# Kernel optimization log

Measured on AMD Instinct MI355X. Metric: run time of the kernel, lower is better.

The kernel has to match this reference:

```python
import jax, jax.numpy as jnp
import numpy as np

T = 8
TAU = 2.0       # spikingjelly LIFNode default tau
VTH = 1.0       # default v_threshold
ALPHA = 2.0     # surrogate.ATan alpha
EPS = 1e-5      # BatchNorm eps


@jax.custom_vjp
def spike_fn(x):
    # Heaviside with ATan surrogate gradient
    return (x >= 0.0).astype(x.dtype)

def _spike_fwd(x):
    return (x >= 0.0).astype(x.dtype), x

def _spike_bwd(x, g):
    sg = (ALPHA / 2.0) / (1.0 + (jnp.pi / 2.0 * ALPHA * x) ** 2)
    return (g * sg,)

spike_fn.defvjp(_spike_fwd, _spike_bwd)


def lif(x_seq):
    """Multi-step LIF over leading time axis. decay_input=True, hard reset to 0, detach_reset."""
    def step(v, x):
        v = v + (x - v) / TAU            # charge
        s = spike_fn(v - VTH)            # fire (surrogate grad)
        v = v * (1.0 - jax.lax.stop_gradient(s))  # detached hard reset to v_reset=0
        return v, s
    _, s_seq = jax.lax.scan(step, jnp.zeros_like(x_seq[0]), x_seq)
    return s_seq


def conv2d(x, w, b, stride):
    y = jax.lax.conv_general_dilated(x, w, (stride, stride), 'VALID',
                                     dimension_numbers=('NCHW', 'OIHW', 'NCHW'))
    return y + b[None, :, None, None]


def batchnorm(x, g, b):
    # training-mode BN over merged (T*B, H, W) axes, matching step_mode='m' BatchNorm2d
    m = x.mean((0, 2, 3), keepdims=True)
    v = x.var((0, 2, 3), keepdims=True)
    return g[None, :, None, None] * (x - m) * jax.lax.rsqrt(v + EPS) + b[None, :, None, None]


def setup_inputs() -> dict:
    key = jax.random.key(0)
    ks = jax.random.split(key, 12)
    def w_init(k, shape):
        fan_in = int(np.prod(shape[1:]))
        return jax.random.normal(k, shape, dtype=jnp.float32) / np.sqrt(fan_in)
    x = jax.random.normal(ks[0], (128, 4, 84, 84), dtype=jnp.float32)
    return {
        'x': x,
        'conv1_w': w_init(ks[1], (32, 4, 8, 8)),  'conv1_b': jnp.zeros((32,), jnp.float32),
        'bn1_g': jnp.ones((32,), jnp.float32),    'bn1_b': jnp.zeros((32,), jnp.float32),
        'conv2_w': w_init(ks[2], (64, 32, 4, 4)), 'conv2_b': jnp.zeros((64,), jnp.float32),
        'bn2_g': jnp.ones((64,), jnp.float32),    'bn2_b': jnp.zeros((64,), jnp.float32),
        'conv3_w': w_init(ks[3], (64, 64, 3, 3)), 'conv3_b': jnp.zeros((64,), jnp.float32),
        'bn3_g': jnp.ones((64,), jnp.float32),    'bn3_b': jnp.zeros((64,), jnp.float32),
        'fc1_w': w_init(ks[4], (512, 3136)),      'fc1_b': jnp.zeros((512,), jnp.float32),
        'fco_w': w_init(ks[5], (2, 512)),         'fco_b': jnp.zeros((2,), jnp.float32),
    }


def reference(x, conv1_w, conv1_b, bn1_g, bn1_b, conv2_w, conv2_b, bn2_g, bn2_b,
              conv3_w, conv3_b, bn3_g, bn3_b, fc1_w, fc1_b, fco_w, fco_b):
    B = x.shape[0]
    # replicate input over T timesteps; fold T into batch for conv/BN (step_mode='m')
    xs = jnp.broadcast_to(x, (T,) + x.shape).reshape((T * B,) + x.shape[1:])

    h = batchnorm(conv2d(xs, conv1_w, conv1_b, 4), bn1_g, bn1_b)   # [TB,32,20,20]
    s = lif(h.reshape((T, B) + h.shape[1:]))
    h = s.reshape((T * B,) + s.shape[2:])

    h = batchnorm(conv2d(h, conv2_w, conv2_b, 2), bn2_g, bn2_b)    # [TB,64,9,9]
    s = lif(h.reshape((T, B) + h.shape[1:]))
    h = s.reshape((T * B,) + s.shape[2:])

    h = batchnorm(conv2d(h, conv3_w, conv3_b, 1), bn3_g, bn3_b)    # [TB,64,7,7]
    s = lif(h.reshape((T, B) + h.shape[1:]))                        # [T,B,64,7,7]

    feat = s.reshape(T, B, -1)                                      # [T,B,3136]
    hid = lif(jnp.einsum('tbi,oi->tbo', feat, fc1_w) + fc1_b)       # [T,B,512]
    out_seq = jnp.einsum('tbo,ko->tbk', hid, fco_w) + fco_b         # [T,B,2]
    return out_seq.mean(0)                                          # [B,2]
```

## Files before the change

### kernel.cpp

```cpp
#include <hip/hip_runtime.h>
#include <cstdint>
#include <cstddef>

#define TT 8

#define E2_ELEMS (128*64*81)
#define E3_ELEMS (128*64*49)

typedef __attribute__((ext_vector_type(8))) short short8;
typedef __attribute__((ext_vector_type(4))) float f32x4;

__global__ void prep_all(const float* __restrict__ w1, const float* __restrict__ w2,
                         const float* __restrict__ w3, float* __restrict__ wT1,
                         __bf16* __restrict__ w2f, __bf16* __restrict__ w3f) {
  int i = blockIdx.x * 256 + threadIdx.x;
  if (i < 8192) {
    int oc = i >> 8, pos = i & 255;
    wT1[(oc >> 4) * 4096 + pos * 16 + (oc & 15)] = w1[oc * 256 + pos];
  } else if (i < 106496) {
    int v = i - 8192;
    int j    = v & 7;
    int oc   = (v >> 3) & 63;
    int quad = (v >> 9) & 3;
    int ksg  = (v >> 11) & 15;
    int term = v >> 15;
    int k = ksg * 32 + quad * 8 + j;
    int ci = k >> 4, kpos = k & 15;
    float w = w2[oc * 512 + ci * 16 + kpos];
    float hf = (float)(__bf16)w;
    float r1 = w - hf;
    float mf = (float)(__bf16)r1;
    float r2 = r1 - mf;
    w2f[v] = (term == 0) ? (__bf16)w : (term == 1) ? (__bf16)r1 : (__bf16)r2;
  } else if (i < 217088) {
    int v = i - 106496;
    int j    = v & 7;
    int oc   = (v >> 3) & 63;
    int quad = (v >> 9) & 3;
    int tk   = v >> 11;
    int term = tk / 18, kstep = tk % 18;
    int k = kstep * 32 + quad * 8 + j;
    int pos = k >> 6, ci = k & 63;
    float w = w3[oc * 576 + ci * 9 + pos];
    float hf = (float)(__bf16)w;
    float r1 = w - hf;
    float mf = (float)(__bf16)r1;
    float r2 = r1 - mf;
    w3f[v] = (term == 0) ? (__bf16)w : (term == 1) ? (__bf16)r1 : (__bf16)r2;
  }
}

__global__ __launch_bounds__(256) void prep_wff(const float* __restrict__ w,
                                                __bf16* __restrict__ wf) {
  __shared__ float tile[12544];
  int oc0 = blockIdx.x * 32;
  int ci0 = blockIdx.y * 8;
  int tid = threadIdx.x;
  for (int f = tid; f < 12544; f += 256) {
    int oc_l = f / 392, r = f - oc_l * 392;
    tile[f] = w[(size_t)(oc0 + oc_l) * 3136 + ci0 * 49 + r];
  }
  __syncthreads();
  int squad = (ci0 & 31) >> 3;
  int sadd  = ci0 >> 5;
  for (int g = tid; g < 1568; g += 256) {
    int pos = g >> 5, oc_l = g & 31;
    union { __bf16 h[8]; uint4 u; } T0, T1, T2;
    #pragma unroll
    for (int j = 0; j < 8; j++) {
      float wv = tile[oc_l * 392 + j * 49 + pos];
      float hf = (float)(__bf16)wv;
      float r1 = wv - hf;
      float mf = (float)(__bf16)r1;
      float r2 = r1 - mf;
      T0.h[j] = (__bf16)wv; T1.h[j] = (__bf16)r1; T2.h[j] = (__bf16)r2;
    }
    int s = pos * 2 + sadd;
    size_t b0 = (((size_t)s * 4 + squad) * 512 + oc0 + oc_l) * 8;
    *(uint4*)(wf + b0)           = T0.u;
    *(uint4*)(wf + b0 + 1605632) = T1.u;
    *(uint4*)(wf + b0 + 3211264) = T2.u;
  }
}

__global__ __launch_bounds__(128) void k_conv1(const float* __restrict__ x,
                                               const float* __restrict__ wT,
                                               const float* __restrict__ bias,
                                               float* __restrict__ out,
                                               float* __restrict__ pout) {
  __shared__ float xt[8064];
  int tid = threadIdx.x;
  int img = blockIdx.x >> 2;
  int q   = blockIdx.x & 3;
  int och = blockIdx.y;
  float4* dst = (float4*)xt;
  #pragma unroll
  for (int ci = 0; ci < 4; ci++) {
    const float4* s4 = (const float4*)(x + (size_t)img * 28224 + ci * 7056 + q * 1680);
    for (int i = tid; i < 504; i += 128) dst[ci * 504 + i] = s4[i];
  }
  __syncthreads();
  bool active = tid < 100;
  int oyl = tid / 20, ox = tid % 20;
  float acc[16];
  #pragma unroll
  for (int j = 0; j < 16; j++) acc[j] = 0.f;
  if (active) {
    int xb0 = oyl * 336 + ox * 4;
    const float* wh = wT + och * 4096;
    #pragma unroll 1
    for (int ci = 0; ci < 4; ci++) {
      #pragma unroll 1
      for (int ky = 0; ky < 8; ky++) {
        const float* xr = xt + ci * 2016 + xb0 + ky * 84;
        float4 xa  = *(const float4*)xr;
        float4 xbv = *(const float4*)(xr + 4);
        const float* wr = wh + (ci * 8 + ky) * 128;
        float xs[8] = {xa.x, xa.y, xa.z, xa.w, xbv.x, xbv.y, xbv.z, xbv.w};
        #pragma unroll
        for (int kx = 0; kx < 8; kx++) {
          #pragma unroll
          for (int j = 0; j < 16; j++)
            acc[j] = fmaf(xs[kx], wr[kx * 16 + j], acc[j]);
        }
      }
    }
  }
  __syncthreads();
  size_t obase = (size_t)img * 12800 + och * 6400 + (q * 5 + oyl) * 20 + ox;
  #pragma unroll
  for (int j = 0; j < 16; j++) {
    float v = 0.f;
    if (active) {
      v = acc[j] + bias[och * 16 + j];
      out[obase + j * 400] = v;
    }
    xt[j * 128 + tid] = v;
    xt[2048 + j * 128 + tid] = v * v;
  }
  __syncthreads();
  for (int off = 64; off > 0; off >>= 1) {
    if (tid < off) {
      #pragma unroll
      for (int j = 0; j < 16; j++) {
        xt[j * 128 + tid] += xt[j * 128 + tid + off];
        xt[2048 + j * 128 + tid] += xt[2048 + j * 128 + tid + off];
      }
    }
    __syncthreads();
  }
  if (tid < 16) {
    pout[(och * 16 + tid) * 512 + blockIdx.x] = xt[tid * 128];
    pout[16384 + (och * 16 + tid) * 512 + blockIdx.x] = xt[2048 + tid * 128];
  }
}

__global__ void k_bnfinal2(const float* __restrict__ pin, int sqoff, float n,
                           float* __restrict__ meanArr, float* __restrict__ rstdArr) {
  __shared__ float l0[256], l1[256];
  int c = blockIdx.x, tid = threadIdx.x;
  l0[tid] = pin[c * 512 + tid] + pin[c * 512 + tid + 256];
  l1[tid] = pin[sqoff + c * 512 + tid] + pin[sqoff + c * 512 + tid + 256];
  __syncthreads();
  for (int k = 128; k > 0; k >>= 1) {
    if (tid < k) { l0[tid] += l0[tid + k]; l1[tid] += l1[tid + k]; }
    __syncthreads();
  }
  if (tid == 0) {
    float m = l0[0] / n;
    float var = l1[0] / n - m * m;
    meanArr[c] = m;
    rstdArr[c] = rsqrtf(var + 1e-5f);
  }
}

__global__ void k_lif1b(const float* __restrict__ h, const float* __restrict__ mean,
                        const float* __restrict__ rstd, const float* __restrict__ g,
                        const float* __restrict__ bb, uint32_t* __restrict__ sout) {
  int idx = blockIdx.x * 256 + threadIdx.x;
  int ic = idx / 20;
  int ci = ic & 31;
  const float* hp = h + (size_t)idx * 20;
  float gm = g[ci], mm = mean[ci], rs = rstd[ci], bc = bb[ci];
  float xv[20];
  #pragma unroll
  for (int j4 = 0; j4 < 5; j4++) {
    float4 hv = ((const float4*)hp)[j4];
    xv[j4 * 4 + 0] = gm * (hv.x - mm) * rs + bc;
    xv[j4 * 4 + 1] = gm * (hv.y - mm) * rs + bc;
    xv[j4 * 4 + 2] = gm * (hv.z - mm) * rs + bc;
    xv[j4 * 4 + 3] = gm * (hv.w - mm) * rs + bc;
  }
  float v[20];
  #pragma unroll
  for (int j = 0; j < 20; j++) v[j] = 0.f;
  #pragma unroll
  for (int t = 0; t < TT; t++) {
    uint32_t w = 0;
    #pragma unroll
    for (int j = 0; j < 20; j++) {
      v[j] = v[j] + (xv[j] - v[j]) * 0.5f;
      uint32_t s = (v[j] >= 1.0f);
      w |= s << j;
      if (s) v[j] = 0.f;
    }
    sout[t * 81920 + idx] = w;
  }
}

__global__ __launch_bounds__(256) void k_conv2m(const uint32_t* __restrict__ s1b,
                                                const __bf16* __restrict__ wf,
                                                const float* __restrict__ bias,
                                                float* __restrict__ out,
                                                float* __restrict__ pout) {
  __shared__ uint32_t sp[1280];
  __shared__ uint4 wl4[3072];
  __bf16* wl = (__bf16*)wl4;
  int tid = threadIdx.x;
  int img0 = blockIdx.x * 2;
  {
    const uint32_t* src = s1b + (size_t)img0 * 640;
    for (int i = tid; i < 1280; i += 256) sp[i] = src[i];
  }
  int wave = tid >> 6, lane = tid & 63;
  int img_local = wave >> 1;
  int nh = wave & 1;
  int l15 = lane & 15, quad = lane >> 4;
  int ci_off = quad >> 1;
  int kyp = (quad & 1) * 2;
  int spb[6], sh[6];
  #pragma unroll
  for (int mt = 0; mt < 6; mt++) {
    int px = mt * 16 + l15;
    if (px > 80) px = 80;
    int oy = px / 9, ox = px - oy * 9;
    sh[mt]  = ox * 2;
    spb[mt] = img_local * 640 + ci_off * 20 + oy * 2 + kyp;
  }
  f32x4 acc[6][2];
  #pragma unroll
  for (int mt = 0; mt < 6; mt++)
    #pragma unroll
    for (int nt = 0; nt < 2; nt++) acc[mt][nt] = (f32x4){0.f, 0.f, 0.f, 0.f};

  for (int kc = 0; kc < 4; kc++) {
    __syncthreads();
    for (int o = tid * 8; o < 24576; o += 2048) {
      int tk = o >> 11;
      int term = tk >> 2, ksl = tk & 3;
      const __bf16* src = wf + (((term * 16 + kc * 4 + ksl)) << 11) + (o & 2047);
      *(uint4*)(wl + o) = *(const uint4*)src;
    }
    __syncthreads();
    #pragma unroll
    for (int ks = 0; ks < 4; ks++) {
      int ksg = kc * 4 + ks;
      short8 a[6];
      #pragma unroll
      for (int mt = 0; mt < 6; mt++) {
        uint32_t w0 = sp[spb[mt] + ksg * 40];
        uint32_t w1 = sp[spb[mt] + ksg * 40 + 1];
        uint32_t n0 = (w0 >> sh[mt]) & 15u;
        uint32_t n1 = (w1 >> sh[mt]) & 15u;
        union { uint32_t u[4]; short8 v; } A;
        A.u[0] = ((n0 & 1u) ? 0x3F80u : 0u) | ((n0 & 2u) ? 0x3F800000u : 0u);
        A.u[1] = ((n0 & 4u) ? 0x3F80u : 0u) | ((n0 & 8u) ? 0x3F800000u : 0u);
        A.u[2] = ((n1 & 1u) ? 0x3F80u : 0u) | ((n1 & 2u) ? 0x3F800000u : 0u);
        A.u[3] = ((n1 & 4u) ? 0x3F80u : 0u) | ((n1 & 8u) ? 0x3F800000u : 0u);
        a[mt] = A.v;
      }
      #pragma unroll
      for (int term = 0; term < 3; term++) {
        int fb = ((term * 4 + ks) << 11) + (quad << 9);
        #pragma unroll
        for (int nt = 0; nt < 2; nt++) {
          short8 b = *(const short8*)(wl + fb + ((((nh << 1) | nt) << 4) + l15) * 8);
          #pragma unroll
          for (int mt = 0; mt < 6; mt++)
            acc[mt][nt] = __builtin_amdgcn_mfma_f32_16x16x32_bf16(a[mt], b, acc[mt][nt], 0, 0, 0);
        }
      }
    }
  }
  float sl[2], sl2[2];
  #pragma unroll
  for (int nt = 0; nt < 2; nt++) {
    sl[nt] = 0.f; sl2[nt] = 0.f;
    int oc = nh * 32 + nt * 16 + l15;
    float bv = bias[oc];
    float* op = out + ((size_t)(img0 + img_local) * 64 + oc) * 81;
    #pragma unroll
    for (int mt = 0; mt < 6; mt++) {
      int pxr = mt * 16 + quad * 4;
      #pragma unroll
      for (int r = 0; r < 4; r++) {
        int px = pxr + r;
        if (px < 81) {
          float v = acc[mt][nt][r] + bv;
          op[px] = v;
          sl[nt] += v; sl2[nt] += v * v;
        }
      }
    }
  }
  __syncthreads();
  float* sred = (float*)wl4;
  #pragma unroll
  for (int nt = 0; nt < 2; nt++) {
    int oc = nh * 32 + nt * 16 + l15;
    int idx = oc * 8 + img_local * 4 + quad;
    sred[idx] = sl[nt];
    sred[512 + idx] = sl2[nt];
  }
  __syncthreads();
  if (tid < 64) {
    float s = 0.f, s2 = 0.f;
    #pragma unroll
    for (int k = 0; k < 8; k++) { s += sred[tid * 8 + k]; s2 += sred[512 + tid * 8 + k]; }
    pout[tid * 512 + blockIdx.x] = s;
    pout[32768 + tid * 512 + blockIdx.x] = s2;
  }
}

__global__ __launch_bounds__(256) void k_lifb2T(const float* __restrict__ h,
                                                const float* __restrict__ mean,
                                                const float* __restrict__ rstd,
                                                const float* __restrict__ g,
                                                const float* __restrict__ bb,
                                                uint32_t* __restrict__ s2T) {
  __shared__ uint32_t sb[288];
  int b = blockIdx.x, half = blockIdx.y;
  int tid = threadIdx.x;
  int c1 = half * 32 + tid / 9, py1 = tid % 9;
  bool has2 = tid < 32;
  int r2 = tid + 256;
  int c2i = half * 32 + r2 / 9, py2 = r2 % 9;
  float gm1 = g[c1], mm1 = mean[c1], rs1 = rstd[c1], bc1 = bb[c1];
  float gm2 = 0.f, mm2 = 0.f, rs2 = 0.f, bc2 = 0.f;
  if (has2) { gm2 = g[c2i]; mm2 = mean[c2i]; rs2 = rstd[c2i]; bc2 = bb[c2i]; }
  float v1[9], v2[9];
  #pragma unroll
  for (int j = 0; j < 9; j++) { v1[j] = 0.f; v2[j] = 0.f; }
  size_t base1 = ((size_t)b * 64 + c1) * 81 + py1 * 9;
  size_t base2 = has2 ? ((size_t)b * 64 + c2i) * 81 + py2 * 9 : base1;
  #pragma unroll 1
  for (int t = 0; t < TT; t++) {
    const float* hp = h + (size_t)t * E2_ELEMS;
    uint32_t w = 0;
    #pragma unroll
    for (int j = 0; j < 9; j++) {
      float xv = gm1 * (hp[base1 + j] - mm1) * rs1 + bc1;
      v1[j] = v1[j] + (xv - v1[j]) * 0.5f;
      uint32_t s = (v1[j] >= 1.0f);
      w |= s << j;
      if (s) v1[j] = 0.f;
    }
    sb[tid] = w;
    if (has2) {
      uint32_t w2 = 0;
      #pragma unroll
      for (int j = 0; j < 9; j++) {
        float xv = gm2 * (hp[base2 + j] - mm2) * rs2 + bc2;
        v2[j] = v2[j] + (xv - v2[j]) * 0.5f;
        uint32_t s = (v2[j] >= 1.0f);
        w2 |= s << j;
        if (s) v2[j] = 0.f;
      }
      sb[r2] = w2;
    }
    __syncthreads();
    if (tid < 81) {
      int r = tid / 9, cpix = tid - r * 9;
      uint32_t wo = 0;
      #pragma unroll
      for (int ci = 0; ci < 32; ci++)
        wo |= ((sb[ci * 9 + r] >> cpix) & 1u) << ci;
      s2T[(size_t)(t * 128 + b) * 162 + tid * 2 + half] = wo;
    }
    __syncthreads();
  }
}

__global__ __launch_bounds__(256) void k_conv3m(const uint32_t* __restrict__ s2T,
                                                const __bf16* __restrict__ wf,
                                                const float* __restrict__ bias,
                                                float* __restrict__ out,
                                                float* __restrict__ pout) {
  __shared__ uint32_t sp[324];
  __shared__ uint4 wl4[4608];
  __bf16* wl = (__bf16*)wl4;
  int tid = threadIdx.x;
  int img0 = blockIdx.x * 2;
  {
    const uint32_t* src = s2T + (size_t)img0 * 162;
    for (int i = tid; i < 324; i += 256) sp[i] = src[i];
  }
  int wave = tid >> 6, lane = tid & 63;
  int img_local = wave >> 1, nh = wave & 1;
  int l15 = lane & 15, quad = lane >> 4;
  int qsh = quad * 8;
  int base[4];
  #pragma unroll
  for (int mt = 0; mt < 4; mt++) {
    int px = mt * 16 + l15;
    if (px > 48) px = 48;
    int oy = px / 7, ox = px - oy * 7;
    base[mt] = img_local * 162 + (oy * 9 + ox) * 2;
  }
  f32x4 acc[4][2];
  #pragma unroll
  for (int mt = 0; mt < 4; mt++)
    #pragma unroll
    for (int nt = 0; nt < 2; nt++) acc[mt][nt] = (f32x4){0.f, 0.f, 0.f, 0.f};

  #pragma unroll
  for (int kc = 0; kc < 3; kc++) {
    __syncthreads();
    #pragma unroll
    for (int it = 0; it < 18; it++) {
      const __bf16* s = wf + (((it / 6) * 18 + kc * 6 + (it % 6)) << 11) + tid * 8;
      *(uint4*)(wl + (it << 11) + tid * 8) = *(const uint4*)s;
    }
    __syncthreads();
    #pragma unroll
    for (int ksl = 0; ksl < 6; ksl++) {
      int kstep = kc * 6 + ksl;
      int pos = kstep >> 1, cihalf = kstep & 1;
      int ky = pos / 3, kx = pos % 3;
      short8 a[4];
      #pragma unroll
      for (int mt = 0; mt < 4; mt++) {
        uint32_t word = sp[base[mt] + (ky * 9 + kx) * 2 + cihalf];
        uint32_t byt = (word >> qsh) & 255u;
        union { uint32_t u[4]; short8 v; } A;
        A.u[0] = ((byt & 1u)  ? 0x3F80u : 0u) | ((byt & 2u)   ? 0x3F800000u : 0u);
        A.u[1] = ((byt & 4u)  ? 0x3F80u : 0u) | ((byt & 8u)   ? 0x3F800000u : 0u);
        A.u[2] = ((byt & 16u) ? 0x3F80u : 0u) | ((byt & 32u)  ? 0x3F800000u : 0u);
        A.u[3] = ((byt & 64u) ? 0x3F80u : 0u) | ((byt & 128u) ? 0x3F800000u : 0u);
        a[mt] = A.v;
      }
      #pragma unroll
      for (int term = 0; term < 3; term++) {
        int fb = ((term * 6 + ksl) << 11) + (quad << 9);
        #pragma unroll
        for (int nt = 0; nt < 2; nt++) {
          short8 b = *(const short8*)(wl + fb + ((((nh << 1) | nt) << 4) + l15) * 8);
          #pragma unroll
          for (int mt = 0; mt < 4; mt++)
            acc[mt][nt] = __builtin_amdgcn_mfma_f32_16x16x32_bf16(a[mt], b, acc[mt][nt], 0, 0, 0);
        }
      }
    }
  }
  float sl[2], sl2[2];
  #pragma unroll
  for (int nt = 0; nt < 2; nt++) {
    sl[nt] = 0.f; sl2[nt] = 0.f;
    int oc = nh * 32 + nt * 16 + l15;
    float bv = bias[oc];
    float* op = out + ((size_t)(img0 + img_local) * 64 + oc) * 49;
    #pragma unroll
    for (int mt = 0; mt < 4; mt++) {
      int pxr = mt * 16 + quad * 4;
      #pragma unroll
      for (int r = 0; r < 4; r++) {
        int px = pxr + r;
        if (px < 49) {
          float v = acc[mt][nt][r] + bv;
          op[px] = v;
          sl[nt] += v; sl2[nt] += v * v;
        }
      }
    }
  }
  __syncthreads();
  float* sred = (float*)wl4;
  #pragma unroll
  for (int nt = 0; nt < 2; nt++) {
    int oc = nh * 32 + nt * 16 + l15;
    int idx = oc * 8 + img_local * 4 + quad;
    sred[idx] = sl[nt];
    sred[512 + idx] = sl2[nt];
  }
  __syncthreads();
  if (tid < 64) {
    float s = 0.f, s2 = 0.f;
    #pragma unroll
    for (int k = 0; k < 8; k++) { s += sred[tid * 8 + k]; s2 += sred[512 + tid * 8 + k]; }
    pout[tid * 512 + blockIdx.x] = s;
    pout[32768 + tid * 512 + blockIdx.x] = s2;
  }
}

__global__ __launch_bounds__(256) void k_lifb3T(const float* __restrict__ h,
                                                const float* __restrict__ mean,
                                                const float* __restrict__ rstd,
                                                const float* __restrict__ g,
                                                const float* __restrict__ bb,
                                                uint32_t* __restrict__ s3T) {
  __shared__ uint32_t sb[224];
  int b = blockIdx.x, half = blockIdx.y;
  int tid = threadIdx.x;
  bool active = tid < 224;
  int row = active ? tid : 0;
  int c = half * 32 + row / 7, py = row % 7;
  float gm = g[c], mm = mean[c], rs = rstd[c], bc = bb[c];
  float v[7];
  #pragma unroll
  for (int j = 0; j < 7; j++) v[j] = 0.f;
  size_t base = ((size_t)b * 64 + c) * 49 + py * 7;
  #pragma unroll 1
  for (int t = 0; t < TT; t++) {
    const float* hp = h + (size_t)t * E3_ELEMS;
    if (active) {
      uint32_t w = 0;
      #pragma unroll
      for (int j = 0; j < 7; j++) {
        float xv = gm * (hp[base + j] - mm) * rs + bc;
        v[j] = v[j] + (xv - v[j]) * 0.5f;
        uint32_t s = (v[j] >= 1.0f);
        w |= s << j;
        if (s) v[j] = 0.f;
      }
      sb[tid] = w;
    }
    __syncthreads();
    if (tid < 49) {
      int py2 = tid / 7, px = tid - py2 * 7;
      uint32_t wo = 0;
      #pragma unroll
      for (int ci = 0; ci < 32; ci++)
        wo |= ((sb[ci * 7 + py2] >> px) & 1u) << ci;
      s3T[(size_t)(t * 128 + b) * 98 + tid * 2 + half] = wo;
    }
    __syncthreads();
  }
}

__global__ __launch_bounds__(256) void k_fc1m(const uint32_t* __restrict__ s3T,
                                              const __bf16* __restrict__ wf,
                                              float* __restrict__ part) {
  __shared__ uint32_t aS[6272];
  int tid = threadIdx.x;
  int row0 = blockIdx.x * 64;
  int oc0  = blockIdx.y * 32;
  {
    const uint32_t* src = s3T + (size_t)row0 * 98;
    for (int i = tid; i < 6272; i += 256) aS[i] = src[i];
  }
  __syncthreads();
  int wave = tid >> 6, lane = tid & 63;
  int l15 = lane & 15, quad = lane >> 4;
  int qsh = quad * 8;
  f32x4 acc[4][2];
  #pragma unroll
  for (int mt = 0; mt < 4; mt++)
    #pragma unroll
    for (int nt = 0; nt < 2; nt++) acc[mt][nt] = (f32x4){0.f, 0.f, 0.f, 0.f};
  int nIter = (wave < 2) ? 25 : 24;
  #pragma unroll 1
  for (int i = 0; i < nIter; i++) {
    int ks = i * 4 + wave;
    short8 a[4];
    #pragma unroll
    for (int mt = 0; mt < 4; mt++) {
      uint32_t word = aS[(mt * 16 + l15) * 98 + ks];
      uint32_t byt = (word >> qsh) & 255u;
      union { uint32_t u[4]; short8 v; } A;
      A.u[0] = ((byt & 1u)  ? 0x3F80u : 0u) | ((byt & 2u)   ? 0x3F800000u : 0u);
      A.u[1] = ((byt & 4u)  ? 0x3F80u : 0u) | ((byt & 8u)   ? 0x3F800000u : 0u);
      A.u[2] = ((byt & 16u) ? 0x3F80u : 0u) | ((byt & 32u)  ? 0x3F800000u : 0u);
      A.u[3] = ((byt & 64u) ? 0x3F80u : 0u) | ((byt & 128u) ? 0x3F800000u : 0u);
      a[mt] = A.v;
    }
    #pragma unroll
    for (int term = 0; term < 3; term++) {
      size_t fb = ((size_t)((term * 98 + ks) * 4 + quad) * 512 + oc0 + l15) * 8;
      #pragma unroll
      for (int nt = 0; nt < 2; nt++) {
        short8 b = *(const short8*)(wf + fb + nt * 128);
        #pragma unroll
        for (int mt = 0; mt < 4; mt++)
          acc[mt][nt] = __builtin_amdgcn_mfma_f32_16x16x32_bf16(a[mt], b, acc[mt][nt], 0, 0, 0);
      }
    }
  }
  #pragma unroll
  for (int mt = 0; mt < 4; mt++) {
    #pragma unroll
    for (int nt = 0; nt < 2; nt++) {
      int oc = oc0 + nt * 16 + l15;
      #pragma unroll
      for (int r = 0; r < 4; r++) {
        int row = row0 + mt * 16 + quad * 4 + r;
        part[(size_t)wave * 524288 + (size_t)row * 512 + oc] = acc[mt][nt][r];
      }
    }
  }
}

__global__ __launch_bounds__(256) void k_fc1fco(const float* __restrict__ part,
                                                const float* __restrict__ bias,
                                                const float* __restrict__ w,
                                                const float* __restrict__ fcob,
                                                float* __restrict__ out) {
  int b = blockIdx.x, tid = threadIdx.x;
  int o0 = tid, o1 = tid + 256;
  float bv0 = bias[o0], bv1 = bias[o1];
  float v0 = 0.f, v1 = 0.f;
  float a0 = 0.f, a1 = 0.f;
  #pragma unroll
  for (int t = 0; t < TT; t++) {
    int idx0 = t * 65536 + b * 512 + o0;
    float s0 = part[idx0];
    #pragma unroll
    for (int j = 1; j < 4; j++) s0 += part[(size_t)j * 524288 + idx0];
    s0 += bv0;
    v0 = v0 + (s0 - v0) * 0.5f;
    bool sp0 = (v0 >= 1.0f);
    if (sp0) v0 = 0.f;
    int idx1 = idx0 + 256;
    float s1 = part[idx1];
    #pragma unroll
    for (int j = 1; j < 4; j++) s1 += part[(size_t)j * 524288 + idx1];
    s1 += bv1;
    v1 = v1 + (s1 - v1) * 0.5f;
    bool sp1 = (v1 >= 1.0f);
    if (sp1) v1 = 0.f;
    if (sp0) { a0 += w[o0]; a1 += w[512 + o0]; }
    if (sp1) { a0 += w[o1]; a1 += w[512 + o1]; }
  }
  __shared__ float l0[256], l1[256];
  l0[tid] = a0; l1[tid] = a1; __syncthreads();
  for (int k = 128; k > 0; k >>= 1) {
    if (tid < k) { l0[tid] += l0[tid + k]; l1[tid] += l1[tid + k]; }
    __syncthreads();
  }
  if (tid == 0) {
    out[b * 2 + 0] = l0[0] * 0.125f + fcob[0];
    out[b * 2 + 1] = l1[0] * 0.125f + fcob[1];
  }
}

extern "C" void kernel_launch(void* const* d_in, const int* in_sizes, int n_in,
                              void* d_out, int out_size, void* d_ws, size_t ws_size,
                              hipStream_t stream) {
  const float* x    = (const float*)d_in[0];
  const float* c1w  = (const float*)d_in[1];
  const float* c1b  = (const float*)d_in[2];
  const float* bn1g = (const float*)d_in[3];
  const float* bn1b = (const float*)d_in[4];
  const float* c2w  = (const float*)d_in[5];
  const float* c2b  = (const float*)d_in[6];
  const float* bn2g = (const float*)d_in[7];
  const float* bn2b = (const float*)d_in[8];
  const float* c3w  = (const float*)d_in[9];
  const float* c3b  = (const float*)d_in[10];
  const float* bn3g = (const float*)d_in[11];
  const float* bn3b = (const float*)d_in[12];
  const float* fc1w = (const float*)d_in[13];
  const float* fc1b = (const float*)d_in[14];
  const float* fcow = (const float*)d_in[15];
  const float* fcob = (const float*)d_in[16];
  float* out = (float*)d_out;

  char* ws = (char*)d_ws;
  float*    h1     = (float*)(ws + 0);
  uint32_t* s1bits = (uint32_t*)(ws + 6553600);
  float*    h2     = (float*)(ws + 19660800);
  float*    h3     = (float*)(ws + 46202880);
  __bf16*   w2f    = (__bf16*)(ws + 60882944);
  __bf16*   w3f    = (__bf16*)(ws + 61079552);
  uint32_t* s2T    = (uint32_t*)(ws + 61300736);
  float*    wT1    = (float*)(ws + 62390272);
  float*    st     = (float*)(ws + 64880640);
  __bf16*   wff    = (__bf16*)(ws + 67108864);
  float*    f1part = (float*)(ws + 76742656);
  uint32_t* s3T    = (uint32_t*)(ws + 85131264);
  float*    bnpart = (float*)(ws + 85532672);

  prep_all   <<<848, 256, 0, stream>>>(c1w, c2w, c3w, wT1, w2f, w3f);
  prep_wff   <<<dim3(16, 8), 256, 0, stream>>>(fc1w, wff);
  k_conv1    <<<dim3(512, 2), 128, 0, stream>>>(x, wT1, c1b, h1, bnpart);
  k_bnfinal2 <<<32, 256, 0, stream>>>(bnpart, 16384, 51200.f, st, st + 32);
  k_lif1b    <<<320, 256, 0, stream>>>(h1, st, st + 32, bn1g, bn1b, s1bits);

  k_conv2m   <<<512, 256, 0, stream>>>(s1bits, w2f, c2b, h2, bnpart);
  k_bnfinal2 <<<64, 256, 0, stream>>>(bnpart, 32768, 82944.f, st + 64, st + 128);
  k_lifb2T   <<<dim3(128, 2), 256, 0, stream>>>(h2, st + 64, st + 128, bn2g, bn2b, s2T);

  k_conv3m   <<<512, 256, 0, stream>>>(s2T, w3f, c3b, h3, bnpart);
  k_bnfinal2 <<<64, 256, 0, stream>>>(bnpart, 32768, 50176.f, st + 192, st + 256);
  k_lifb3T   <<<dim3(128, 2), 256, 0, stream>>>(h3, st + 192, st + 256, bn3g, bn3b, s3T);

  k_fc1m     <<<dim3(16, 16), 256, 0, stream>>>(s3T, wff, f1part);
  k_fc1fco   <<<128, 256, 0, stream>>>(f1part, fc1b, fcow, fcob, out);
}
```

Before: 251.1 us.

## Use direct global-to-LDS loads, prefetch LIF inputs, reduce fc1 partials in-block

The conv2 and conv3 weight staging now uses global_load_lds, so data goes straight into LDS without passing through registers. The LIF kernels for layers 2 and 3 prefetch the next timestep's activations into registers and use a lighter barrier macro. fc1 now splits output channels into 16-wide tiles across twice as many blocks and sums the four waves' partial results in shared memory. It writes one summed tensor instead of four partial buffers, so the final kernel reads less and uses weights held in registers. These changes add register pressure and more fc1 blocks that re-read the A tile.

```diff
diff --git a/kernel.cpp b/kernel.cpp
--- a/kernel.cpp
+++ b/kernel.cpp
@@ -9,6 +9,14 @@
 
 typedef __attribute__((ext_vector_type(8))) short short8;
 typedef __attribute__((ext_vector_type(4))) float f32x4;
+
+#define BAR_LDS() do { asm volatile("s_waitcnt lgkmcnt(0)" ::: "memory"); \
+                       __builtin_amdgcn_s_barrier(); } while (0)
+
+__device__ __forceinline__ void gld_lds16(const void* g, void* l) {
+  __builtin_amdgcn_global_load_lds((const __attribute__((address_space(1))) void*)g,
+                                   (__attribute__((address_space(3))) void*)l, 16, 0, 0);
+}
 
 __global__ void prep_all(const float* __restrict__ w1, const float* __restrict__ w2,
                          const float* __restrict__ w3, float* __restrict__ wT1,
@@ -249,7 +257,7 @@
       int tk = o >> 11;
       int term = tk >> 2, ksl = tk & 3;
       const __bf16* src = wf + (((term * 16 + kc * 4 + ksl)) << 11) + (o & 2047);
-      *(uint4*)(wl + o) = *(const uint4*)src;
+      gld_lds16(src, wl + o);
     }
     __syncthreads();
     #pragma unroll
@@ -343,13 +351,32 @@
   for (int j = 0; j < 9; j++) { v1[j] = 0.f; v2[j] = 0.f; }
   size_t base1 = ((size_t)b * 64 + c1) * 81 + py1 * 9;
   size_t base2 = has2 ? ((size_t)b * 64 + c2i) * 81 + py2 * 9 : base1;
+  float c1v[9], c2v[9];
+  {
+    const float* hp = h;
+    #pragma unroll
+    for (int j = 0; j < 9; j++) c1v[j] = hp[base1 + j];
+    if (has2) {
+      #pragma unroll
+      for (int j = 0; j < 9; j++) c2v[j] = hp[base2 + j];
+    }
+  }
   #pragma unroll 1
   for (int t = 0; t < TT; t++) {
-    const float* hp = h + (size_t)t * E2_ELEMS;
+    float n1v[9], n2v[9];
+    if (t < TT - 1) {
+      const float* hp = h + (size_t)(t + 1) * E2_ELEMS;
+      #pragma unroll
+      for (int j = 0; j < 9; j++) n1v[j] = hp[base1 + j];
+      if (has2) {
+        #pragma unroll
+        for (int j = 0; j < 9; j++) n2v[j] = hp[base2 + j];
+      }
+    }
     uint32_t w = 0;
     #pragma unroll
     for (int j = 0; j < 9; j++) {
-      float xv = gm1 * (hp[base1 + j] - mm1) * rs1 + bc1;
+      float xv = gm1 * (c1v[j] - mm1) * rs1 + bc1;
       v1[j] = v1[j] + (xv - v1[j]) * 0.5f;
       uint32_t s = (v1[j] >= 1.0f);
       w |= s << j;
@@ -360,7 +387,7 @@
       uint32_t w2 = 0;
       #pragma unroll
       for (int j = 0; j < 9; j++) {
-        float xv = gm2 * (hp[base2 + j] - mm2) * rs2 + bc2;
+        float xv = gm2 * (c2v[j] - mm2) * rs2 + bc2;
         v2[j] = v2[j] + (xv - v2[j]) * 0.5f;
         uint32_t s = (v2[j] >= 1.0f);
         w2 |= s << j;
@@ -368,7 +395,7 @@
       }
       sb[r2] = w2;
     }
-    __syncthreads();
+    BAR_LDS();
     if (tid < 81) {
       int r = tid / 9, cpix = tid - r * 9;
       uint32_t wo = 0;
@@ -377,7 +404,15 @@
         wo |= ((sb[ci * 9 + r] >> cpix) & 1u) << ci;
       s2T[(size_t)(t * 128 + b) * 162 + tid * 2 + half] = wo;
     }
-    __syncthreads();
+    BAR_LDS();
+    if (t < TT - 1) {
+      #pragma unroll
+      for (int j = 0; j < 9; j++) c1v[j] = n1v[j];
+      if (has2) {
+        #pragma unroll
+        for (int j = 0; j < 9; j++) c2v[j] = n2v[j];
+      }
+    }
   }
 }
 
@@ -419,7 +454,7 @@
     #pragma unroll
     for (int it = 0; it < 18; it++) {
       const __bf16* s = wf + (((it / 6) * 18 + kc * 6 + (it % 6)) << 11) + tid * 8;
-      *(uint4*)(wl + (it << 11) + tid * 8) = *(const uint4*)s;
+      gld_lds16(s, wl + (it << 11) + tid * 8);
     }
     __syncthreads();
     #pragma unroll
@@ -509,14 +544,24 @@
   #pragma unroll
   for (int j = 0; j < 7; j++) v[j] = 0.f;
   size_t base = ((size_t)b * 64 + c) * 49 + py * 7;
+  float cv[7];
+  if (active) {
+    #pragma unroll
+    for (int j = 0; j < 7; j++) cv[j] = h[base + j];
+  }
   #pragma unroll 1
   for (int t = 0; t < TT; t++) {
-    const float* hp = h + (size_t)t * E3_ELEMS;
+    float nv[7];
+    if (active && t < TT - 1) {
+      const float* hp = h + (size_t)(t + 1) * E3_ELEMS;
+      #pragma unroll
+      for (int j = 0; j < 7; j++) nv[j] = hp[base + j];
+    }
     if (active) {
       uint32_t w = 0;
       #pragma unroll
       for (int j = 0; j < 7; j++) {
-        float xv = gm * (hp[base + j] - mm) * rs + bc;
+        float xv = gm * (cv[j] - mm) * rs + bc;
         v[j] = v[j] + (xv - v[j]) * 0.5f;
         uint32_t s = (v[j] >= 1.0f);
         w |= s << j;
@@ -524,7 +569,7 @@
       }
       sb[tid] = w;
     }
-    __syncthreads();
+    BAR_LDS();
     if (tid < 49) {
       int py2 = tid / 7, px = tid - py2 * 7;
       uint32_t wo = 0;
@@ -533,17 +578,21 @@
         wo |= ((sb[ci * 7 + py2] >> px) & 1u) << ci;
       s3T[(size_t)(t * 128 + b) * 98 + tid * 2 + half] = wo;
     }
-    __syncthreads();
+    BAR_LDS();
+    if (active && t < TT - 1) {
+      #pragma unroll
+      for (int j = 0; j < 7; j++) cv[j] = nv[j];
+    }
   }
 }
 
 __global__ __launch_bounds__(256) void k_fc1m(const uint32_t* __restrict__ s3T,
                                               const __bf16* __restrict__ wf,
-                                              float* __restrict__ part) {
+                                              float* __restrict__ f1) {
   __shared__ uint32_t aS[6272];
   int tid = threadIdx.x;
   int row0 = blockIdx.x * 64;
-  int oc0  = blockIdx.y * 32;
+  int oc0  = blockIdx.y * 16;
   {
     const uint32_t* src = s3T + (size_t)row0 * 98;
     for (int i = tid; i < 6272; i += 256) aS[i] = src[i];
@@ -552,13 +601,11 @@
   int wave = tid >> 6, lane = tid & 63;
   int l15 = lane & 15, quad = lane >> 4;
   int qsh = quad * 8;
-  f32x4 acc[4][2];
-  #pragma unroll
-  for (int mt = 0; mt < 4; mt++)
-    #pragma unroll
-    for (int nt = 0; nt < 2; nt++) acc[mt][nt] = (f32x4){0.f, 0.f, 0.f, 0.f};
+  f32x4 acc[4];
+  #pragma unroll
+  for (int mt = 0; mt < 4; mt++) acc[mt] = (f32x4){0.f, 0.f, 0.f, 0.f};
   int nIter = (wave < 2) ? 25 : 24;
-  #pragma unroll 1
+  #pragma unroll 2
   for (int i = 0; i < nIter; i++) {
     int ks = i * 4 + wave;
     short8 a[4];
@@ -576,30 +623,36 @@
     #pragma unroll
     for (int term = 0; term < 3; term++) {
       size_t fb = ((size_t)((term * 98 + ks) * 4 + quad) * 512 + oc0 + l15) * 8;
-      #pragma unroll
-      for (int nt = 0; nt < 2; nt++) {
-        short8 b = *(const short8*)(wf + fb + nt * 128);
-        #pragma unroll
-        for (int mt = 0; mt < 4; mt++)
-          acc[mt][nt] = __builtin_amdgcn_mfma_f32_16x16x32_bf16(a[mt], b, acc[mt][nt], 0, 0, 0);
-      }
-    }
-  }
-  #pragma unroll
-  for (int mt = 0; mt < 4; mt++) {
-    #pragma unroll
-    for (int nt = 0; nt < 2; nt++) {
-      int oc = oc0 + nt * 16 + l15;
-      #pragma unroll
-      for (int r = 0; r < 4; r++) {
-        int row = row0 + mt * 16 + quad * 4 + r;
-        part[(size_t)wave * 524288 + (size_t)row * 512 + oc] = acc[mt][nt][r];
-      }
-    }
-  }
-}
-
-__global__ __launch_bounds__(256) void k_fc1fco(const float* __restrict__ part,
+      short8 b = *(const short8*)(wf + fb);
+      #pragma unroll
+      for (int mt = 0; mt < 4; mt++)
+        acc[mt] = __builtin_amdgcn_mfma_f32_16x16x32_bf16(a[mt], b, acc[mt], 0, 0, 0);
+    }
+  }
+  __syncthreads();
+  float* red = (float*)aS;
+  #pragma unroll
+  for (int mt = 0; mt < 4; mt++)
+    #pragma unroll
+    for (int r = 0; r < 4; r++)
+      red[(wave * 64 + lane) * 17 + mt * 4 + r] = acc[mt][r];
+  __syncthreads();
+  #pragma unroll
+  for (int k = 0; k < 4; k++) {
+    int oi = tid + k * 256;
+    int row_l = oi >> 4, oc_l = oi & 15;
+    int mt = row_l >> 4, rem = row_l & 15;
+    int q2 = rem >> 2, r = rem & 3;
+    int ln = q2 * 16 + oc_l;
+    float s = red[(0 * 64 + ln) * 17 + mt * 4 + r];
+    s += red[(1 * 64 + ln) * 17 + mt * 4 + r];
+    s += red[(2 * 64 + ln) * 17 + mt * 4 + r];
+    s += red[(3 * 64 + ln) * 17 + mt * 4 + r];
+    f1[(size_t)(row0 + row_l) * 512 + oc0 + oc_l] = s;
+  }
+}
+
+__global__ __launch_bounds__(256) void k_fc1fco(const float* __restrict__ f1,
                                                 const float* __restrict__ bias,
                                                 const float* __restrict__ w,
                                                 const float* __restrict__ fcob,
@@ -607,28 +660,28 @@
   int b = blockIdx.x, tid = threadIdx.x;
   int o0 = tid, o1 = tid + 256;
   float bv0 = bias[o0], bv1 = bias[o1];
+  float w00 = w[o0], w10 = w[512 + o0];
+  float w01 = w[o1], w11 = w[512 + o1];
+  float x0[TT], x1[TT];
+  #pragma unroll
+  for (int t = 0; t < TT; t++) {
+    x0[t] = f1[(size_t)(t * 128 + b) * 512 + o0];
+    x1[t] = f1[(size_t)(t * 128 + b) * 512 + o1];
+  }
   float v0 = 0.f, v1 = 0.f;
   float a0 = 0.f, a1 = 0.f;
   #pragma unroll
   for (int t = 0; t < TT; t++) {
-    int idx0 = t * 65536 + b * 512 + o0;
-    float s0 = part[idx0];
-    #pragma unroll
-    for (int j = 1; j < 4; j++) s0 += part[(size_t)j * 524288 + idx0];
-    s0 += bv0;
+    float s0 = x0[t] + bv0;
     v0 = v0 + (s0 - v0) * 0.5f;
     bool sp0 = (v0 >= 1.0f);
     if (sp0) v0 = 0.f;
-    int idx1 = idx0 + 256;
-    float s1 = part[idx1];
-    #pragma unroll
-    for (int j = 1; j < 4; j++) s1 += part[(size_t)j * 524288 + idx1];
-    s1 += bv1;
+    float s1 = x1[t] + bv1;
     v1 = v1 + (s1 - v1) * 0.5f;
     bool sp1 = (v1 >= 1.0f);
     if (sp1) v1 = 0.f;
-    if (sp0) { a0 += w[o0]; a1 += w[512 + o0]; }
-    if (sp1) { a0 += w[o1]; a1 += w[512 + o1]; }
+    if (sp0) { a0 += w00; a1 += w10; }
+    if (sp1) { a0 += w01; a1 += w11; }
   }
   __shared__ float l0[256], l1[256];
   l0[tid] = a0; l1[tid] = a1; __syncthreads();
@@ -675,7 +728,7 @@
   float*    wT1    = (float*)(ws + 62390272);
   float*    st     = (float*)(ws + 64880640);
   __bf16*   wff    = (__bf16*)(ws + 67108864);
-  float*    f1part = (float*)(ws + 76742656);
+  float*    f1sum  = (float*)(ws + 76742656);
   uint32_t* s3T    = (uint32_t*)(ws + 85131264);
   float*    bnpart = (float*)(ws + 85532672);
 
@@ -693,6 +746,6 @@
   k_bnfinal2 <<<64, 256, 0, stream>>>(bnpart, 32768, 50176.f, st + 192, st + 256);
   k_lifb3T   <<<dim3(128, 2), 256, 0, stream>>>(h3, st + 192, st + 256, bn3g, bn3b, s3T);
 
-  k_fc1m     <<<dim3(16, 16), 256, 0, stream>>>(s3T, wff, f1part);
-  k_fc1fco   <<<128, 256, 0, stream>>>(f1part, fc1b, fcow, fcob, out);
-}
+  k_fc1m     <<<dim3(16, 32), 256, 0, stream>>>(s3T, wff, f1sum);
+  k_fc1fco   <<<128, 256, 0, stream>>>(f1sum, fc1b, fcow, fcob, out);
+}
```

New measurement: 247.0 us. Within noise of the previous version (-1.7%).
